# Kernel optimization log

Hardware: AMD Instinct MI355X
Metric: run time of the kernel (lower is better)

## Reference

```python
import jax, jax.numpy as jnp
import numpy as np

N = 100000
E = 1600000
DIN = 256
DOUT = 64


def setup_inputs() -> dict:
    key = jax.random.key(0)
    ks = jax.random.split(key, 12)
    s = 1.0 / np.sqrt(DIN)
    so = 1.0 / np.sqrt(DOUT)
    return {
        "x": jax.random.normal(ks[0], (N, DIN), dtype=jnp.float32),
        "edge_index": jax.random.randint(ks[1], (2, E), 0, N, dtype=jnp.int32),
        "W_hp": jax.random.uniform(ks[2], (DIN, DOUT), jnp.float32, -s, s),
        "b_hp": jnp.zeros((DOUT,), jnp.float32),
        "W_lp": jax.random.uniform(ks[3], (DIN, DOUT), jnp.float32, -s, s),
        "b_lp": jnp.zeros((DOUT,), jnp.float32),
        "W_i": jax.random.uniform(ks[4], (DIN, DOUT), jnp.float32, -s, s),
        "b_i": jnp.zeros((DOUT,), jnp.float32),
        "w_h": jax.random.uniform(ks[5], (DOUT, 1), jnp.float32, -so, so),
        "b_h": jnp.zeros((1,), jnp.float32),
        "w_l": jax.random.uniform(ks[6], (DOUT, 1), jnp.float32, -so, so),
        "b_l": jnp.zeros((1,), jnp.float32),
        "w_i2": jax.random.uniform(ks[7], (DOUT, 1), jnp.float32, -so, so),
        "b_i2": jnp.zeros((1,), jnp.float32),
    }


def _gcn_norm(edge_index, n):
    # add self loops, symmetric GCN normalization
    ar = jnp.arange(n, dtype=edge_index.dtype)
    src = jnp.concatenate([edge_index[0], ar])
    dst = jnp.concatenate([edge_index[1], ar])
    deg = jax.ops.segment_sum(jnp.ones_like(dst, dtype=jnp.float32), dst, num_segments=n)
    dinv = jnp.where(deg > 0, jax.lax.rsqrt(jnp.maximum(deg, 1e-12)), 0.0)
    norm = dinv[src] * dinv[dst]  # [E+N]
    return src, dst, norm


def reference(x, edge_index, W_hp, b_hp, W_lp, b_lp, W_i, b_i,
              w_h, b_h, w_l, b_l, w_i2, b_i2):
    n = x.shape[0]
    src, dst, norm = _gcn_norm(edge_index, n)

    def prop(h):  # Ahat @ h via gather-scale-scatter
        return jax.ops.segment_sum(h[src] * norm[:, None], dst, num_segments=n)

    # three ACM-GCN filter branches
    xw_hp = x @ W_hp + b_hp
    H_hp = jax.nn.relu(xw_hp - prop(xw_hp))      # high-pass: (I - Ahat) X W
    H_lp = jax.nn.relu(prop(x @ W_lp + b_lp))    # low-pass:  Ahat X W
    H_i = jax.nn.relu(x @ W_i + b_i)             # identity:  X W

    # per-node sigmoid gates (mix=False path)
    a_h = jax.nn.sigmoid(H_hp @ w_h + b_h)[:, 0]
    a_l = jax.nn.sigmoid(H_lp @ w_l + b_l)[:, 0]
    a_i = jax.nn.sigmoid(H_i @ w_i2 + b_i2)[:, 0]

    # diag(alpha) @ H == broadcasted row scaling (same math, no NxN diag)
    out = a_h[:, None] * H_hp + a_l[:, None] * H_lp + a_i[:, None] * H_i
    return jax.nn.log_softmax(out, axis=1)
```

## Files before the change

kernel.cpp:

```cpp
#include <hip/hip_runtime.h>
#include <hip/hip_bf16.h>
#include <hip/hip_fp16.h>
#include <math.h>

#define DIN 256
#define DOUT 64

#define BKT_CAP 1408
#define C1_CAP 36864
#define CH1 4096
#define CH2 4096
#define NB2_PER 9

typedef __attribute__((ext_vector_type(8))) short bfrag8;
typedef __attribute__((ext_vector_type(4))) float ffrag4;
typedef __fp16 fp16x2 __attribute__((ext_vector_type(2)));

#define AS1 __attribute__((address_space(1)))
#define AS3 __attribute__((address_space(3)))

__device__ inline unsigned short f2bf(float f) {
    union { float f; unsigned u; } v; v.f = f;
    unsigned r = v.u + 0x7FFF + ((v.u >> 16) & 1);
    return (unsigned short)(r >> 16);
}
__device__ inline unsigned cvt2(float a, float b) {
    unsigned r;
    asm("v_cvt_pk_bf16_f32 %0, %1, %2" : "=v"(r) : "v"(a), "v"(b));
    return r;
}

__device__ inline float wave_sum(float v) {
    #pragma unroll
    for (int off = 32; off > 0; off >>= 1) v += __shfl_xor(v, off, 64);
    return v;
}
__device__ inline float wave_max(float v) {
    #pragma unroll
    for (int off = 32; off > 0; off >>= 1) v = fmaxf(v, __shfl_xor(v, off, 64));
    return v;
}

__device__ inline void gload16(const void* g, void* l) {
    __builtin_amdgcn_global_load_lds((const AS1 void*)g, (AS3 void*)l, 16, 0, 0);
}

union HU { unsigned u; __half2 h; };

__device__ inline void prew_body(int id, const float* __restrict__ Whp,
                                 const float* __restrict__ Wlp,
                                 const float* __restrict__ Wi,
                                 unsigned* __restrict__ wt) {
    if (id >= 8 * 192 * 4) return;
    int p = id & 3;
    int col = (id >> 2) % 192;
    int kci = id / (192 * 4);
    int s = p ^ ((col >> 1) & 3);
    int m = col >> 6, c = col & 63;
    const float* W = (m == 0) ? Whp : ((m == 1) ? Wlp : Wi);
    int k0 = kci * 32 + s * 4;
    unsigned o0 = (unsigned)f2bf(W[(k0 + 0) * 64 + c]) | ((unsigned)f2bf(W[(k0 + 1) * 64 + c]) << 16);
    unsigned o1 = (unsigned)f2bf(W[(k0 + 2) * 64 + c]) | ((unsigned)f2bf(W[(k0 + 3) * 64 + c]) << 16);
    unsigned o2 = (unsigned)f2bf(W[(k0 + 16) * 64 + c]) | ((unsigned)f2bf(W[(k0 + 17) * 64 + c]) << 16);
    unsigned o3 = (unsigned)f2bf(W[(k0 + 18) * 64 + c]) | ((unsigned)f2bf(W[(k0 + 19) * 64 + c]) << 16);
    uint4 v; v.x = o0; v.y = o1; v.z = o2; v.w = o3;
    *(uint4*)&wt[(size_t)id * 4] = v;
}

__global__ __launch_bounds__(256) void k_bin1(
    const int* __restrict__ src, const int* __restrict__ dst, int E,
    int* __restrict__ gcnt1, unsigned* __restrict__ cwords,
    const float* __restrict__ Whp, const float* __restrict__ Wlp,
    const float* __restrict__ Wi, unsigned* __restrict__ wt) {
    __shared__ int hist[4][64];
    __shared__ int roff[4][64];
    __shared__ int loff[64], gb[64];
    __shared__ unsigned words[CH1];
    __shared__ unsigned char aux[CH1];
    int t = threadIdx.x;
    int rep = t & 3;
    int base = blockIdx.x * CH1;
    int nloc = E - base;
    if (nloc > CH1) nloc = CH1;
    if (nloc < 0) nloc = 0;
    if (t < 64) { hist[0][t] = 0; hist[1][t] = 0; hist[2][t] = 0; hist[3][t] = 0; }
    __syncthreads();
    unsigned myw[16];
    short myr[16];
    signed char myb[16];
    #pragma unroll
    for (int i = 0; i < 16; ++i) {
        int idx = i * 256 + t;
        myb[i] = -1;
        if (idx < nloc) {
            int s = src[base + idx], d = dst[base + idx];
            int b = d >> 11;
            myw[i] = (unsigned)s | ((unsigned)(d & 2047) << 17);
            myb[i] = (signed char)b;
            myr[i] = (short)atomicAdd(&hist[rep][b], 1);
        }
    }
    __syncthreads();
    if (t < 64) {
        int run = 0;
        #pragma unroll
        for (int r = 0; r < 4; ++r) { roff[r][t] = run; run += hist[r][t]; }
        hist[0][t] = run;
    }
    __syncthreads();
    if (t == 0) {
        int run = 0;
        for (int i2 = 0; i2 < 64; ++i2) { loff[i2] = run; run += hist[0][i2]; }
    }
    __syncthreads();
    if (t < 64) {
        int c = hist[0][t];
        gb[t] = c ? atomicAdd(&gcnt1[t], c) : 0;
    }
    __syncthreads();
    #pragma unroll
    for (int i = 0; i < 16; ++i) {
        if (myb[i] >= 0) {
            int b = myb[i];
            int pos = loff[b] + roff[rep][b] + myr[i];
            words[pos] = myw[i];
            aux[pos] = (unsigned char)b;
        }
    }
    __syncthreads();
    for (int j = t; j < nloc; j += 256) {
        int b = aux[j];
        int g = gb[b] + (j - loff[b]);
        if (g < C1_CAP) cwords[(size_t)b * C1_CAP + g] = words[j];
    }
    if (blockIdx.x < 24) prew_body(blockIdx.x * 256 + t, Whp, Wlp, Wi, wt);
}

__global__ __launch_bounds__(256) void k_bin2(
    const int* __restrict__ gcnt1, const unsigned* __restrict__ cwords,
    int* __restrict__ gcnt2, unsigned* __restrict__ bwords,
    int* __restrict__ cnt, int N) {
    __shared__ int hist[32], loff[32], gb[32];
    __shared__ int hist2k[2048];
    __shared__ unsigned words[CH2];
    __shared__ unsigned char aux[CH2];
    int t = threadIdx.x;
    int b = blockIdx.x / NB2_PER, j = blockIdx.x % NB2_PER;
    int tot = gcnt1[b];
    if (tot > C1_CAP) tot = C1_CAP;
    int base = j * CH2;
    int nloc = tot - base;
    if (nloc <= 0) return;
    if (nloc > CH2) nloc = CH2;
    if (t < 32) hist[t] = 0;
    for (int i = t; i < 2048; i += 256) hist2k[i] = 0;
    __syncthreads();
    unsigned myw[16];
    short myr[16];
    signed char myf[16];
    const unsigned* cw = cwords + (size_t)b * C1_CAP + base;
    #pragma unroll
    for (int i = 0; i < 16; ++i) {
        int idx = i * 256 + t;
        myf[i] = -1;
        if (idx < nloc) {
            unsigned w = cw[idx];
            int ld = (int)(w >> 17);
            int f = ld >> 6;
            myw[i] = (w & 0x1FFFF) | ((unsigned)(ld & 63) << 17);
            myf[i] = (signed char)f;
            myr[i] = (short)atomicAdd(&hist[f], 1);
            atomicAdd(&hist2k[ld], 1);
        }
    }
    __syncthreads();
    if (t == 0) {
        int run = 0;
        for (int i2 = 0; i2 < 32; ++i2) { loff[i2] = run; run += hist[i2]; }
    }
    __syncthreads();
    if (t < 32) {
        int c = hist[t];
        gb[t] = c ? atomicAdd(&gcnt2[b * 32 + t], c) : 0;
    }
    __syncthreads();
    #pragma unroll
    for (int i = 0; i < 16; ++i) {
        if (myf[i] >= 0) {
            int pos = loff[myf[i]] + myr[i];
            words[pos] = myw[i];
            aux[pos] = (unsigned char)myf[i];
        }
    }
    __syncthreads();
    for (int j2 = t; j2 < nloc; j2 += 256) {
        int f = aux[j2];
        int g = gb[f] + (j2 - loff[f]);
        if (g < BKT_CAP) bwords[(size_t)(b * 32 + f) * BKT_CAP + g] = words[j2];
    }
    int nbase = b * 2048;
    for (int i = t; i < 2048; i += 256) {
        int c = hist2k[i];
        if (c && nbase + i < N) atomicAdd(&cnt[nbase + i], c);
    }
}

__global__ __launch_bounds__(256) void k_gemm(
    const float* __restrict__ x, int N,
    const unsigned* __restrict__ wt,
    const float* __restrict__ bhp, const float* __restrict__ blp,
    const float* __restrict__ bi, const int* __restrict__ cnt,
    unsigned* __restrict__ xws, __half* __restrict__ xwi) {
    __shared__ __attribute__((aligned(16))) float Al[128 * 32];
    __shared__ __attribute__((aligned(16))) unsigned short Bl[192 * 32];
    int t = threadIdx.x;
    int wave = t >> 6, lane = t & 63;
    int l15 = lane & 15, lhi = lane >> 4;
    int row0 = blockIdx.x * 128;

    ffrag4 acc[2][12];
    #pragma unroll
    for (int mf = 0; mf < 2; ++mf)
        #pragma unroll
        for (int nf = 0; nf < 12; ++nf)
            acc[mf][nf] = (ffrag4){0.f, 0.f, 0.f, 0.f};

    int arow[4], achk[4];
    #pragma unroll
    for (int i = 0; i < 4; ++i) {
        int off = i * 4096 + t * 16;
        int r = off >> 7;
        int cp = (off >> 4) & 7;
        arow[i] = row0 + r < N ? row0 + r : N - 1;
        achk[i] = cp ^ (r & 7);
    }

    for (int kci = 0; kci < 8; ++kci) {
        #pragma unroll
        for (int i = 0; i < 4; ++i)
            gload16(x + (size_t)arow[i] * DIN + kci * 32 + achk[i] * 4,
                    (char*)Al + i * 4096 + wave * 1024);
        #pragma unroll
        for (int i = 0; i < 3; ++i)
            gload16(wt + (size_t)kci * 3072 + ((i * 4096 + t * 16) >> 2),
                    (char*)Bl + i * 4096 + wave * 1024);
        __syncthreads();

        union { bfrag8 v; unsigned u[4]; } af[2];
        #pragma unroll
        for (int mf = 0; mf < 2; ++mf) {
            int row = wave * 32 + mf * 16 + l15;
            int p1 = lhi ^ (row & 7);
            float4 lo = ((const float4*)Al)[row * 8 + p1];
            float4 hi = ((const float4*)Al)[row * 8 + (p1 ^ 4)];
            af[mf].u[0] = cvt2(lo.x, lo.y);
            af[mf].u[1] = cvt2(lo.z, lo.w);
            af[mf].u[2] = cvt2(hi.x, hi.y);
            af[mf].u[3] = cvt2(hi.z, hi.w);
        }
        bfrag8 bfr[12];
        #pragma unroll
        for (int nf = 0; nf < 12; ++nf) {
            int col = nf * 16 + l15;
            int p = lhi ^ ((col >> 1) & 3);
            bfr[nf] = *((const bfrag8*)Bl + col * 4 + p);
        }
        #pragma unroll
        for (int mf = 0; mf < 2; ++mf)
            #pragma unroll
            for (int nf = 0; nf < 12; ++nf)
                acc[mf][nf] = __builtin_amdgcn_mfma_f32_16x16x32_bf16(
                    af[mf].v, bfr[nf], acc[mf][nf], 0, 0, 0);
        __syncthreads();
    }

    #pragma unroll
    for (int mf = 0; mf < 2; ++mf) {
        #pragma unroll
        for (int nf = 0; nf < 4; ++nf) {
            int col = nf * 16 + l15;
            float bh_ = bhp[col], bl_ = blp[col], bi_ = bi[col];
            #pragma unroll
            for (int r = 0; r < 4; ++r) {
                int grow = row0 + wave * 32 + mf * 16 + lhi * 4 + r;
                if (grow >= N) continue;
                float dv = rsqrtf((float)cnt[grow] + 1.f);
                float hp = (acc[mf][nf][r] + bh_) * dv;
                float lp = (acc[mf][nf + 4][r] + bl_) * dv;
                union { fp16x2 p; unsigned u; } pu;
                pu.p = __builtin_amdgcn_cvt_pkrtz(hp, lp);
                xws[(size_t)grow * 64 + col] = pu.u;
                xwi[(size_t)grow * 64 + col] = __float2half(acc[mf][nf + 8][r] + bi_);
            }
        }
    }
}

__global__ __launch_bounds__(256) void k_bagg(
    const int* __restrict__ gcnt2, const unsigned* __restrict__ bwords,
    const unsigned* __restrict__ xws, const __half* __restrict__ xwi,
    const float* __restrict__ wh, const float* __restrict__ bh,
    const float* __restrict__ wl, const float* __restrict__ bl,
    const float* __restrict__ wi2, const float* __restrict__ bi2,
    float* __restrict__ out, int N) {
    __shared__ unsigned sorted[1024];
    __shared__ int h2[32], lo2[32], sc[32];
    int t = threadIdx.x, bb = blockIdx.x;
    int b = bb >> 1, half = bb & 1;
    int n0 = b * 64 + half * 32;
    if (n0 >= N) return;
    int cntE = gcnt2[b];
    if (cntE > BKT_CAP) cntE = BKT_CAP;
    if (t < 32) h2[t] = 0;
    __syncthreads();
    unsigned mw[6];
    short ml[6], mr[6];
    #pragma unroll
    for (int i = 0; i < 6; ++i) {
        int idx = i * 256 + t;
        ml[i] = -1;
        if (idx < cntE) {
            unsigned w = bwords[(size_t)b * BKT_CAP + idx];
            int ld = (int)(w >> 17);
            if ((ld >> 5) == half) {
                int l5 = ld & 31;
                mw[i] = (w & 0x1FFFF) << 8;
                ml[i] = (short)l5;
                mr[i] = (short)atomicAdd(&h2[l5], 1);
            }
        }
    }
    __syncthreads();
    if (t < 32) sc[t] = h2[t];
    __syncthreads();
    for (int off = 1; off < 32; off <<= 1) {
        int x = (t < 32 && t >= off) ? sc[t - off] : 0;
        __syncthreads();
        if (t < 32) sc[t] += x;
        __syncthreads();
    }
    if (t < 32) lo2[t] = sc[t] - h2[t];
    __syncthreads();
    #pragma unroll
    for (int i = 0; i < 6; ++i)
        if (ml[i] >= 0) {
            int pos = lo2[ml[i]] + mr[i];
            if (pos < 1024) sorted[pos] = mw[i];
        }
    __syncthreads();

    int wave = t >> 6, lane = t & 63;
    int h = lane >> 5, f2 = lane & 31;
    const unsigned laneoff = (unsigned)(f2 * 8);
    const char* bp = (const char*)xws;
    float wh0 = wh[f2 * 2], wh1 = wh[f2 * 2 + 1];
    float wl0 = wl[f2 * 2], wl1 = wl[f2 * 2 + 1];
    float wi0 = wi2[f2 * 2], wi1 = wi2[f2 * 2 + 1];
    float bhv = bh[0], blv = bl[0], biv = bi2[0];
    for (int ni = 0; ni < 8; ++ni) {
        int ln = wave * 8 + ni;
        int node = n0 + ln;
        if (node >= N) break;
        int c = h2[ln], e0 = lo2[ln], e1 = e0 + c;
        if (e1 > 1024) e1 = 1024;
        unsigned long long us = *(const unsigned long long*)(bp + ((unsigned)node << 8) + laneoff);
        HU z; z.u = 0;
        __half2 acc0 = z.h, acc1 = z.h;
        int e = e0;
        for (; e + 16 <= e1; e += 16) {
            unsigned long long v[8];
            #pragma unroll
            for (int k = 0; k < 8; ++k)
                v[k] = *(const unsigned long long*)(bp + (sorted[e + 2 * k + h] + laneoff));
            #pragma unroll
            for (int k = 0; k < 8; ++k) {
                HU a, bq;
                a.u = (unsigned)v[k];
                bq.u = (unsigned)(v[k] >> 32);
                acc0 = __hadd2(acc0, a.h);
                acc1 = __hadd2(acc1, bq.h);
            }
        }
        if (e + 8 <= e1) {
            unsigned long long v[4];
            #pragma unroll
            for (int k = 0; k < 4; ++k)
                v[k] = *(const unsigned long long*)(bp + (sorted[e + 2 * k + h] + laneoff));
            #pragma unroll
            for (int k = 0; k < 4; ++k) {
                HU a, bq;
                a.u = (unsigned)v[k];
                bq.u = (unsigned)(v[k] >> 32);
                acc0 = __hadd2(acc0, a.h);
                acc1 = __hadd2(acc1, bq.h);
            }
            e += 8;
        }
        if (e + 4 <= e1) {
            unsigned long long v[2];
            #pragma unroll
            for (int k = 0; k < 2; ++k)
                v[k] = *(const unsigned long long*)(bp + (sorted[e + 2 * k + h] + laneoff));
            #pragma unroll
            for (int k = 0; k < 2; ++k) {
                HU a, bq;
                a.u = (unsigned)v[k];
                bq.u = (unsigned)(v[k] >> 32);
                acc0 = __hadd2(acc0, a.h);
                acc1 = __hadd2(acc1, bq.h);
            }
            e += 4;
        }
        for (; e < e1; e += 2) {
            int ei = e + h;
            if (ei < e1) {
                unsigned long long v = *(const unsigned long long*)(bp + (sorted[ei] + laneoff));
                HU a, bq;
                a.u = (unsigned)v;
                bq.u = (unsigned)(v >> 32);
                acc0 = __hadd2(acc0, a.h);
                acc1 = __hadd2(acc1, bq.h);
            }
        }
        HU c0, c1;
        c0.h = acc0; c0.u = __shfl_xor(c0.u, 32, 64);
        c1.h = acc1; c1.u = __shfl_xor(c1.u, 32, 64);
        acc0 = __hadd2(acc0, c0.h);
        acc1 = __hadd2(acc1, c1.h);
        float s_h0 = __low2float(acc0), s_l0 = __high2float(acc0);
        float s_h1 = __low2float(acc1), s_l1 = __high2float(acc1);
        float fc = (float)c + 1.f;
        float dv = rsqrtf(fc), sq = sqrtf(fc);
        HU q0, q1;
        q0.u = (unsigned)us; q1.u = (unsigned)(us >> 32);
        float xh0 = __low2float(q0.h), xl0 = __high2float(q0.h);
        float xh1 = __low2float(q1.h), xl1 = __high2float(q1.h);
        float Hh0 = fmaxf(xh0 * sq - dv * (s_h0 + xh0), 0.f);
        float Hh1 = fmaxf(xh1 * sq - dv * (s_h1 + xh1), 0.f);
        float Hl0 = fmaxf(dv * (s_l0 + xl0), 0.f);
        float Hl1 = fmaxf(dv * (s_l1 + xl1), 0.f);
        HU qi;
        qi.u = *(const unsigned*)((const char*)xwi + ((size_t)node * 128) + f2 * 4);
        float Hi0 = fmaxf(__low2float(qi.h), 0.f);
        float Hi1 = fmaxf(__high2float(qi.h), 0.f);
        float zh = 0.5f * wave_sum(Hh0 * wh0 + Hh1 * wh1) + bhv;
        float zl = 0.5f * wave_sum(Hl0 * wl0 + Hl1 * wl1) + blv;
        float zi = 0.5f * wave_sum(Hi0 * wi0 + Hi1 * wi1) + biv;
        float ah = 1.f / (1.f + expf(-zh));
        float al = 1.f / (1.f + expf(-zl));
        float ai = 1.f / (1.f + expf(-zi));
        float o0 = ah * Hh0 + al * Hl0 + ai * Hi0;
        float o1 = ah * Hh1 + al * Hl1 + ai * Hi1;
        float mx = wave_max(fmaxf(o0, o1));
        float ss = 0.5f * wave_sum(expf(o0 - mx) + expf(o1 - mx));
        float lse = mx + logf(ss);
        if (h == 0) {
            float2 r; r.x = o0 - lse; r.y = o1 - lse;
            *(float2*)&out[(size_t)node * 64 + f2 * 2] = r;
        }
    }
}

extern "C" void kernel_launch(void* const* d_in, const int* in_sizes, int n_in,
                              void* d_out, int out_size, void* d_ws, size_t ws_size,
                              hipStream_t stream) {
    const float* x   = (const float*)d_in[0];
    const int*   ei  = (const int*)d_in[1];
    const float* Whp = (const float*)d_in[2];
    const float* bhp = (const float*)d_in[3];
    const float* Wlp = (const float*)d_in[4];
    const float* blp = (const float*)d_in[5];
    const float* Wi  = (const float*)d_in[6];
    const float* bi  = (const float*)d_in[7];
    const float* wh  = (const float*)d_in[8];
    const float* bh  = (const float*)d_in[9];
    const float* wl  = (const float*)d_in[10];
    const float* bl  = (const float*)d_in[11];
    const float* wi2 = (const float*)d_in[12];
    const float* bi2 = (const float*)d_in[13];
    float* out = (float*)d_out;

    int N = in_sizes[0] / DIN;
    int E = in_sizes[1] / 2;
    const int* src = ei;
    const int* dst = ei + E;
    int nc = (N + 2047) >> 11;
    int nbuck2 = nc * 32;

    char* w = (char*)d_ws;
    size_t off = 0;
    auto alloc = [&](size_t bytes) {
        void* p = w + off;
        off += (bytes + 255) & ~size_t(255);
        return p;
    };
    int*      cnt    = (int*)alloc((size_t)N * 4);
    int*      gcnt1  = (int*)alloc(64 * 4);
    int*      gcnt2  = (int*)alloc((size_t)nbuck2 * 4);
    size_t    zero_end = off;
    unsigned* cwords = (unsigned*)alloc((size_t)nc * C1_CAP * 4);
    unsigned* bwords = (unsigned*)alloc((size_t)nbuck2 * BKT_CAP * 4);
    unsigned* xws    = (unsigned*)alloc((size_t)N * 64 * 4);
    __half*   xwi    = (__half*)alloc((size_t)N * 64 * 2);
    unsigned* wt     = (unsigned*)alloc((size_t)8 * 192 * 4 * 16);
    (void)ws_size; (void)n_in; (void)out_size;

    hipError_t e0 = hipMemsetAsync(cnt, 0, zero_end, stream); (void)e0;
    k_bin1<<<(E + CH1 - 1) / CH1, 256, 0, stream>>>(src, dst, E, gcnt1, cwords,
                                                    Whp, Wlp, Wi, wt);
    k_bin2<<<nc * NB2_PER, 256, 0, stream>>>(gcnt1, cwords, gcnt2, bwords, cnt, N);
    k_gemm<<<(N + 127) / 128, 256, 0, stream>>>(x, N, wt, bhp, blp, bi, cnt,
                                                xws, xwi);
    k_bagg<<<nbuck2 * 2, 256, 0, stream>>>(gcnt2, bwords, xws, xwi,
                                           wh, bh, wl, bl, wi2, bi2, out, N);
}
```

Before: 147.8 us.

## Use wave-shuffle prefix scans, halve bin1 chunk, split half2 accumulators

Replaces serial single-thread and barrier-heavy shared-memory prefix sums in k_bin1, k_bin2 and k_bagg with wave-level __shfl_up scans, which removes several __syncthreads and serial loops. k_bin1 chunk size is halved, giving twice as many blocks with fewer edges each, which raises parallelism but also doubles the global atomic traffic on the bucket counters. The aggregation loop now uses two independent half2 accumulator chains per output to shorten the add dependency chain, which slightly changes fp16 summation order.

```diff
diff --git a/kernel.cpp b/kernel.cpp
--- a/kernel.cpp
+++ b/kernel.cpp
@@ -8,7 +8,7 @@
 
 #define BKT_CAP 1408
 #define C1_CAP 36864
-#define CH1 4096
+#define CH1 2048
 #define CH2 4096
 #define NB2_PER 9
 
@@ -85,11 +85,11 @@
     if (nloc < 0) nloc = 0;
     if (t < 64) { hist[0][t] = 0; hist[1][t] = 0; hist[2][t] = 0; hist[3][t] = 0; }
     __syncthreads();
-    unsigned myw[16];
-    short myr[16];
-    signed char myb[16];
-    #pragma unroll
-    for (int i = 0; i < 16; ++i) {
+    unsigned myw[8];
+    short myr[8];
+    signed char myb[8];
+    #pragma unroll
+    for (int i = 0; i < 8; ++i) {
         int idx = i * 256 + t;
         myb[i] = -1;
         if (idx < nloc) {
@@ -105,21 +105,19 @@
         int run = 0;
         #pragma unroll
         for (int r = 0; r < 4; ++r) { roff[r][t] = run; run += hist[r][t]; }
-        hist[0][t] = run;
-    }
-    __syncthreads();
-    if (t == 0) {
-        int run = 0;
-        for (int i2 = 0; i2 < 64; ++i2) { loff[i2] = run; run += hist[0][i2]; }
-    }
-    __syncthreads();
-    if (t < 64) {
-        int c = hist[0][t];
-        gb[t] = c ? atomicAdd(&gcnt1[t], c) : 0;
-    }
-    __syncthreads();
-    #pragma unroll
-    for (int i = 0; i < 16; ++i) {
+        int v = run;
+        int x = v;
+        #pragma unroll
+        for (int off = 1; off < 64; off <<= 1) {
+            int y = __shfl_up(x, off, 64);
+            if (t >= off) x += y;
+        }
+        loff[t] = x - v;
+        gb[t] = v ? atomicAdd(&gcnt1[t], v) : 0;
+    }
+    __syncthreads();
+    #pragma unroll
+    for (int i = 0; i < 8; ++i) {
         if (myb[i] >= 0) {
             int b = myb[i];
             int pos = loff[b] + roff[rep][b] + myr[i];
@@ -174,14 +172,16 @@
         }
     }
     __syncthreads();
-    if (t == 0) {
-        int run = 0;
-        for (int i2 = 0; i2 < 32; ++i2) { loff[i2] = run; run += hist[i2]; }
-    }
-    __syncthreads();
     if (t < 32) {
-        int c = hist[t];
-        gb[t] = c ? atomicAdd(&gcnt2[b * 32 + t], c) : 0;
+        int v = hist[t];
+        int x = v;
+        #pragma unroll
+        for (int off = 1; off < 32; off <<= 1) {
+            int y = __shfl_up(x, off, 64);
+            if (t >= off) x += y;
+        }
+        loff[t] = x - v;
+        gb[t] = v ? atomicAdd(&gcnt2[b * 32 + t], v) : 0;
     }
     __syncthreads();
     #pragma unroll
@@ -304,7 +304,7 @@
     const float* __restrict__ wi2, const float* __restrict__ bi2,
     float* __restrict__ out, int N) {
     __shared__ unsigned sorted[1024];
-    __shared__ int h2[32], lo2[32], sc[32];
+    __shared__ int h2[32], lo2[32];
     int t = threadIdx.x, bb = blockIdx.x;
     int b = bb >> 1, half = bb & 1;
     int n0 = b * 64 + half * 32;
@@ -331,15 +331,16 @@
         }
     }
     __syncthreads();
-    if (t < 32) sc[t] = h2[t];
-    __syncthreads();
-    for (int off = 1; off < 32; off <<= 1) {
-        int x = (t < 32 && t >= off) ? sc[t - off] : 0;
-        __syncthreads();
-        if (t < 32) sc[t] += x;
-        __syncthreads();
-    }
-    if (t < 32) lo2[t] = sc[t] - h2[t];
+    if (t < 32) {
+        int v = h2[t];
+        int x = v;
+        #pragma unroll
+        for (int off = 1; off < 32; off <<= 1) {
+            int y = __shfl_up(x, off, 64);
+            if (t >= off) x += y;
+        }
+        lo2[t] = x - v;
+    }
     __syncthreads();
     #pragma unroll
     for (int i = 0; i < 6; ++i)
@@ -365,7 +366,7 @@
         if (e1 > 1024) e1 = 1024;
         unsigned long long us = *(const unsigned long long*)(bp + ((unsigned)node << 8) + laneoff);
         HU z; z.u = 0;
-        __half2 acc0 = z.h, acc1 = z.h;
+        __half2 a0a = z.h, a0b = z.h, a1a = z.h, a1b = z.h;
         int e = e0;
         for (; e + 16 <= e1; e += 16) {
             unsigned long long v[8];
@@ -373,12 +374,12 @@
             for (int k = 0; k < 8; ++k)
                 v[k] = *(const unsigned long long*)(bp + (sorted[e + 2 * k + h] + laneoff));
             #pragma unroll
-            for (int k = 0; k < 8; ++k) {
-                HU a, bq;
-                a.u = (unsigned)v[k];
-                bq.u = (unsigned)(v[k] >> 32);
-                acc0 = __hadd2(acc0, a.h);
-                acc1 = __hadd2(acc1, bq.h);
+            for (int k = 0; k < 8; k += 2) {
+                HU a, bq, c2, d2;
+                a.u = (unsigned)v[k];      bq.u = (unsigned)(v[k] >> 32);
+                c2.u = (unsigned)v[k + 1]; d2.u = (unsigned)(v[k + 1] >> 32);
+                a0a = __hadd2(a0a, a.h);  a1a = __hadd2(a1a, bq.h);
+                a0b = __hadd2(a0b, c2.h); a1b = __hadd2(a1b, d2.h);
             }
         }
         if (e + 8 <= e1) {
@@ -387,12 +388,12 @@
             for (int k = 0; k < 4; ++k)
                 v[k] = *(const unsigned long long*)(bp + (sorted[e + 2 * k + h] + laneoff));
             #pragma unroll
-            for (int k = 0; k < 4; ++k) {
-                HU a, bq;
-                a.u = (unsigned)v[k];
-                bq.u = (unsigned)(v[k] >> 32);
-                acc0 = __hadd2(acc0, a.h);
-                acc1 = __hadd2(acc1, bq.h);
+            for (int k = 0; k < 4; k += 2) {
+                HU a, bq, c2, d2;
+                a.u = (unsigned)v[k];      bq.u = (unsigned)(v[k] >> 32);
+                c2.u = (unsigned)v[k + 1]; d2.u = (unsigned)(v[k + 1] >> 32);
+                a0a = __hadd2(a0a, a.h);  a1a = __hadd2(a1a, bq.h);
+                a0b = __hadd2(a0b, c2.h); a1b = __hadd2(a1b, d2.h);
             }
             e += 8;
         }
@@ -401,14 +402,11 @@
             #pragma unroll
             for (int k = 0; k < 2; ++k)
                 v[k] = *(const unsigned long long*)(bp + (sorted[e + 2 * k + h] + laneoff));
-            #pragma unroll
-            for (int k = 0; k < 2; ++k) {
-                HU a, bq;
-                a.u = (unsigned)v[k];
-                bq.u = (unsigned)(v[k] >> 32);
-                acc0 = __hadd2(acc0, a.h);
-                acc1 = __hadd2(acc1, bq.h);
-            }
+            HU a, bq, c2, d2;
+            a.u = (unsigned)v[0];  bq.u = (unsigned)(v[0] >> 32);
+            c2.u = (unsigned)v[1]; d2.u = (unsigned)(v[1] >> 32);
+            a0a = __hadd2(a0a, a.h);  a1a = __hadd2(a1a, bq.h);
+            a0b = __hadd2(a0b, c2.h); a1b = __hadd2(a1b, d2.h);
             e += 4;
         }
         for (; e < e1; e += 2) {
@@ -418,10 +416,12 @@
                 HU a, bq;
                 a.u = (unsigned)v;
                 bq.u = (unsigned)(v >> 32);
-                acc0 = __hadd2(acc0, a.h);
-                acc1 = __hadd2(acc1, bq.h);
+                a0a = __hadd2(a0a, a.h);
+                a1a = __hadd2(a1a, bq.h);
             }
         }
+        __half2 acc0 = __hadd2(a0a, a0b);
+        __half2 acc1 = __hadd2(a1a, a1b);
         HU c0, c1;
         c0.h = acc0; c0.u = __shfl_xor(c0.u, 32, 64);
         c1.h = acc1; c1.u = __shfl_xor(c1.u, 32, 64);
```

New measurement: 150.7 us. About the same (+1.9%).
